# Optimization experiments

Hardware: AMD Instinct MI355X
Metric: run time of the kernel (lower is better)

Reference implementation:

```python
import jax, jax.numpy as jnp
import numpy as np

TEMP_LEN = 16
TARGET_LEN = 22
DIM = 768
HEADS = 12
B = 16
NT = TEMP_LEN * TEMP_LEN          # 256 template tokens
NG = TARGET_LEN * TARGET_LEN      # 484 target tokens
N = NT + NG                       # 740
POS_HID = 512


def _gaussian_heatmap(center, size, sig=1.0):
    x_axis = np.linspace(0, size[0] - 1, size[0]) - center[0]
    y_axis = np.linspace(0, size[1] - 1, size[1]) - center[1]
    xx, yy = np.meshgrid(x_axis, y_axis)
    return np.exp(-0.5 * (xx ** 2 + yy ** 2) / sig ** 2)


def _bias_index(L):
    # faithful to getBiasIndex (w_len == h_len here)
    coords = np.stack(np.meshgrid(np.arange(L), np.arange(L), indexing='ij'))  # [2,L,L]
    flat = coords.reshape(2, -1)                                               # [2,L*L]
    rel = (flat[:, :, None] - flat[:, None, :]).transpose(1, 2, 0).astype(np.int64)
    rel[:, :, 0] += L - 1
    rel[:, :, 1] += L - 1
    rel[:, :, 0] *= 2 * L - 1
    return rel.sum(-1)  # [L*L, L*L]


def setup_inputs() -> dict:
    key = jax.random.key(0)
    ks = jax.random.split(key, 12)
    f32 = jnp.float32
    x = jax.random.normal(ks[0], (B, N, DIM), dtype=f32)
    temp_q = jax.random.normal(ks[1], (B, NT, DIM), dtype=f32)
    target_q = jax.random.normal(ks[2], (B, NG, DIM), dtype=f32)
    # linear weights stored [in, out] (transposed torch layout)
    w = lambda k, i, o: jax.random.normal(k, (i, o), dtype=f32) * 0.02
    q_w = w(ks[3], DIM, DIM)
    k_w = w(ks[4], DIM, DIM)
    v_w = w(ks[5], DIM, DIM)
    proj_w = w(ks[6], DIM, DIM)
    proj_b = jnp.zeros((DIM,), dtype=f32)
    rpb_table = jax.random.normal(ks[7], ((2 * TARGET_LEN - 1) ** 2, HEADS), dtype=f32) * 0.0002
    rpb_table_temp = jax.random.normal(ks[8], ((2 * TEMP_LEN - 1) ** 2, HEADS), dtype=f32) * 0.0002
    pos_w1 = w(ks[9], 2, POS_HID)
    pos_b1 = jnp.zeros((POS_HID,), dtype=f32)
    pos_w2 = w(ks[10], POS_HID, HEADS)
    pos_b2 = jnp.zeros((HEADS,), dtype=f32)
    # deterministic cross-bias coordinate table (non-learned buffer)
    temp_tab = _gaussian_heatmap((TEMP_LEN // 2, TEMP_LEN // 2), (TEMP_LEN, TEMP_LEN)).astype(np.float32).flatten() \
        + np.linspace(-0.2, 0.2, NT, dtype=np.float32)
    targ_tab = _gaussian_heatmap((TARGET_LEN // 2, TARGET_LEN // 2), (TARGET_LEN, TARGET_LEN)).astype(np.float32).flatten() \
        + np.linspace(-0.2, 0.2, NG, dtype=np.float32)
    # torch.meshgrid default indexing='ij': [2, NT, NG] -> permute(1,2,0) -> [NT,NG,2]
    temp_target = np.stack(np.meshgrid(temp_tab, targ_tab, indexing='ij')).transpose(1, 2, 0)
    target_temp_tab = jnp.asarray(temp_target.transpose(1, 0, 2))  # [NG, NT, 2]
    temp_idx = jnp.asarray(_bias_index(TEMP_LEN))       # [NT, NT] int64
    target_idx = jnp.asarray(_bias_index(TARGET_LEN))   # [NG, NG] int64
    return {
        'x': x, 'temp_q': temp_q, 'target_q': target_q,
        'q_w': q_w, 'k_w': k_w, 'v_w': v_w, 'proj_w': proj_w, 'proj_b': proj_b,
        'rpb_table': rpb_table, 'rpb_table_temp': rpb_table_temp,
        'pos_w1': pos_w1, 'pos_b1': pos_b1, 'pos_w2': pos_w2, 'pos_b2': pos_b2,
        'target_temp_tab': target_temp_tab,
        'temp_idx': temp_idx, 'target_idx': target_idx,
    }


def reference(x, temp_q, target_q, q_w, k_w, v_w, proj_w, proj_b,
              rpb_table, rpb_table_temp, pos_w1, pos_b1, pos_w2, pos_b2,
              target_temp_tab, temp_idx, target_idx):
    Bsz, Ntok, C = x.shape
    H = HEADS
    hd = C // H
    scale = hd ** -0.5

    q_in = jnp.concatenate([temp_q, target_q], axis=1)                 # [B,N,C]
    q = (q_in @ q_w).reshape(Bsz, Ntok, H, hd).transpose(0, 2, 1, 3)   # [B,H,N,hd]
    k = (x @ k_w).reshape(Bsz, Ntok, H, hd).transpose(0, 2, 1, 3)
    v = (x @ v_w).reshape(Bsz, Ntok, H, hd).transpose(0, 2, 1, 3)

    # gathered relative position biases -> [H, Ni, Ni]
    temp_rpb = rpb_table_temp[temp_idx.reshape(-1)].reshape(NT, NT, H).transpose(2, 0, 1)
    targ_rpb = rpb_table[target_idx.reshape(-1)].reshape(NG, NG, H).transpose(2, 0, 1)
    # MLP cross bias: [NG, NT, 2] -> [NG, NT, H] -> [H, NG, NT]
    hid = jax.nn.relu(target_temp_tab @ pos_w1 + pos_b1)
    target_temp_bias = (hid @ pos_w2 + pos_b2).transpose(2, 0, 1)      # [H,NG,NT]
    temp_target_bias = target_temp_bias.transpose(0, 2, 1)             # [H,NT,NG]
    top = jnp.concatenate([temp_rpb, temp_target_bias], axis=2)        # [H,NT,N]
    bot = jnp.concatenate([target_temp_bias, targ_rpb], axis=2)        # [H,NG,N]
    bias = jnp.concatenate([top, bot], axis=1)[None]                   # [1,H,N,N]

    attn = jnp.einsum('bhnd,bhmd->bhnm', q, k) * scale + bias
    attn = jax.nn.softmax(attn, axis=-1)
    out = jnp.einsum('bhnm,bhmd->bhnd', attn, v).transpose(0, 2, 1, 3).reshape(Bsz, Ntok, C)
    return out @ proj_w + proj_b
```

## Files before the change

### kernel.cpp

```cpp
#include <hip/hip_runtime.h>


typedef unsigned short u16;
typedef short bf16x8 __attribute__((ext_vector_type(8)));
typedef float f32x4 __attribute__((ext_vector_type(4)));

#define BSZ   16
#define NTOK  740
#define NTMP  256
#define NTGT  484
#define DIMC  768
#define NHEAD 12
#define HDIM  64
#define MROWS (BSZ*NTOK)
#define SMAX  16.0f

__device__ __forceinline__ float bf2f(u16 u) {
    return __uint_as_float(((unsigned int)u) << 16);
}
__device__ __forceinline__ float bflo(unsigned int u) {
    return __uint_as_float(u << 16);
}
__device__ __forceinline__ float bfhi(unsigned int u) {
    return __uint_as_float(u & 0xffff0000u);
}
__device__ __forceinline__ u16 f2bf(float f) {
    unsigned int u = __float_as_uint(f);
    u += 0x7fffu + ((u >> 16) & 1u);
    return (u16)(u >> 16);
}

__device__ __forceinline__ void gl_lds16(const u16* g, u16* l) {
    __builtin_amdgcn_global_load_lds(
        (const __attribute__((address_space(1))) unsigned int*)(unsigned long long)g,
        (__attribute__((address_space(3))) unsigned int*)(unsigned int)(unsigned long long)l,
        16, 0, 0);
}

__device__ __forceinline__ size_t b2off(int h, int i, int j) {
    return ((size_t)(h * NTOK + i)) * 768 + ((j >> 6) << 6) + ((j & 15) << 2) + ((j >> 4) & 3);
}

#define PREP_CONV 4440
#define PREP_TRW  (PREP_CONV + 576)
#define PREP_DIAG (PREP_TRW + 2220)
#define PREP_ALL  (PREP_DIAG + 484)

__global__ __launch_bounds__(256) void prep_kernel(
    const float* __restrict__ x, const float* __restrict__ tq,
    const float* __restrict__ gq, u16* __restrict__ XB, u16* __restrict__ QB,
    const float* __restrict__ w0, const float* __restrict__ w1,
    const float* __restrict__ w2, const float* __restrict__ w3,
    u16* __restrict__ Wt,
    const float* __restrict__ rpb, const float* __restrict__ rpbt,
    const int* __restrict__ tidx, const int* __restrict__ gidx,
    const float* __restrict__ pw1, const float* __restrict__ pb1,
    const float* __restrict__ pw2, const float* __restrict__ pb2,
    const float* __restrict__ tab, u16* __restrict__ bias)
{
    __shared__ float T[64][65];
    const int blk = blockIdx.x;
    const int tid = threadIdx.x;

    if (blk < PREP_CONV) {
        int c = blk * 256 + tid;
        {
            const float* s = x + (size_t)c * 8;
            float4 p0 = *(const float4*)s, p1 = *(const float4*)(s + 4);
            u16 e[8] = {f2bf(p0.x), f2bf(p0.y), f2bf(p0.z), f2bf(p0.w),
                        f2bf(p1.x), f2bf(p1.y), f2bf(p1.z), f2bf(p1.w)};
            *(uint4*)(XB + (size_t)c * 8) = *(uint4*)e;
        }
        {
            int row = c / 96, cc = (c - row * 96) * 8;
            int b = row / NTOK, n = row - b * NTOK;
            const float* s = (n < NTMP)
                           ? tq + ((size_t)(b * NTMP + n)) * DIMC + cc
                           : gq + ((size_t)(b * NTGT + (n - NTMP))) * DIMC + cc;
            float4 p0 = *(const float4*)s, p1 = *(const float4*)(s + 4);
            u16 e[8] = {f2bf(p0.x), f2bf(p0.y), f2bf(p0.z), f2bf(p0.w),
                        f2bf(p1.x), f2bf(p1.y), f2bf(p1.z), f2bf(p1.w)};
            *(uint4*)(QB + (size_t)row * DIMC + cc) = *(uint4*)e;
        }
    } else if (blk < PREP_TRW) {
        int t = blk - PREP_CONV;
        int z = t / 144, rem = t - z * 144;
        int bx = rem % 12, by = rem / 12;
        const float* src = (z == 0) ? w0 : (z == 1) ? w1 : (z == 2) ? w2 : w3;
        const float scale = (z == 0) ? 0.125f : 1.0f;
        u16* dst = Wt + (size_t)z * DIMC * DIMC;
        int out0 = bx * 64, in0 = by * 64;
        #pragma unroll
        for (int l = 0; l < 4; l++) {
            int u = tid + (l << 8);
            int r = u >> 4, c4 = (u & 15) << 2;
            float4 p = *(const float4*)(src + (size_t)(in0 + r) * DIMC + out0 + c4);
            T[r][c4] = p.x; T[r][c4 + 1] = p.y; T[r][c4 + 2] = p.z; T[r][c4 + 3] = p.w;
        }
        __syncthreads();
        #pragma unroll
        for (int l = 0; l < 2; l++) {
            int u = tid + (l << 8);
            int r = u >> 3, c8 = (u & 7) << 3;
            u16 e[8];
            #pragma unroll
            for (int i = 0; i < 8; i++) e[i] = f2bf(T[c8 + i][r] * scale);
            *(uint4*)(dst + (size_t)(out0 + r) * DIMC + in0 + c8) = *(uint4*)e;
        }
    } else if (blk < PREP_DIAG) {
        int t = blk - PREP_TRW;
        int jb = t % 3, i = t / 3;
        int j = jb * 256 + tid;
        u16 vals[NHEAD];
        if (j >= NTOK) {
            u16 neg = f2bf(-1e30f);
            #pragma unroll
            for (int h = 0; h < NHEAD; h++) vals[h] = neg;
        } else if (i < NTMP && j < NTMP) {
            int idx = tidx[i * NTMP + j];
            #pragma unroll
            for (int h = 0; h < NHEAD; h++) vals[h] = f2bf(rpbt[idx * NHEAD + h]);
        } else if (i >= NTMP && j >= NTMP) {
            int idx = gidx[(i - NTMP) * NTGT + (j - NTMP)];
            #pragma unroll
            for (int h = 0; h < NHEAD; h++) vals[h] = f2bf(rpb[idx * NHEAD + h]);
        } else {
            return;
        }
        #pragma unroll
        for (int h = 0; h < NHEAD; h++) bias[b2off(h, i, j)] = vals[h];
    } else {
        int g = blk - PREP_DIAG;
        int t = tid;
        float a  = tab[(g * NTMP + t) * 2 + 0];
        float bb = tab[(g * NTMP + t) * 2 + 1];
        float acc[NHEAD];
        #pragma unroll
        for (int h = 0; h < NHEAD; h++) acc[h] = pb2[h];
        for (int k = 0; k < 512; k++) {
            float hid = fmaxf(a * pw1[k] + bb * pw1[512 + k] + pb1[k], 0.0f);
            #pragma unroll
            for (int h = 0; h < NHEAD; h++) acc[h] += hid * pw2[k * NHEAD + h];
        }
        #pragma unroll
        for (int h = 0; h < NHEAD; h++) {
            u16 v = f2bf(acc[h]);
            bias[b2off(h, t, NTMP + g)] = v;
            bias[b2off(h, NTMP + g, t)] = v;
        }
    }
}

template<int MODE>
__global__ __launch_bounds__(256) void gemm_bf16(
    const u16* __restrict__ A, const u16* __restrict__ Wt,
    const float* __restrict__ pb, u16* __restrict__ C0,
    u16* __restrict__ C1, float* __restrict__ Cf)
{
    __shared__ __align__(16) u16 As[2][8192];
    __shared__ __align__(16) u16 Bs[2][8192];
    const int tid = threadIdx.x;
    const int lane = tid & 63, w = tid >> 6;
    const int quad = lane >> 4, ln = lane & 15;

    const int gx = gridDim.x;
    const int nwg = gx * (int)gridDim.y;
    const int flat = blockIdx.y * gx + blockIdx.x;
    const int q = nwg >> 3, r = nwg & 7;
    const int xcd = flat & 7, sidx = flat >> 3;
    const int wg = (xcd < r) ? xcd * (q + 1) + sidx
                             : r * (q + 1) + (xcd - r) * q + sidx;
    const int by = wg / gx, bx = wg - by * gx;

    const int m0 = by << 7;
    const int wm = (w >> 1) << 6, wn = (w & 1) << 6;

    const int nn = bx << 7;
    const u16* Wbase = Wt + (size_t)nn * DIMC;
    u16* Cb;
    int col0;
    if (MODE == 1) {
        if (nn < DIMC) { col0 = nn; Cb = C0; }
        else           { col0 = nn - DIMC; Cb = C1; }
    } else {
        col0 = nn; Cb = C0;
    }

    f32x4 acc[4][4];
    #pragma unroll
    for (int i = 0; i < 4; i++)
        #pragma unroll
        for (int j = 0; j < 4; j++)
            acc[i][j] = (f32x4){0.f, 0.f, 0.f, 0.f};

#define STAGE(s, k0) do {                                                     \
    _Pragma("unroll")                                                         \
    for (int l = 0; l < 4; l++) {                                             \
        int f = tid + (l << 8);                                  \
        int c8 = f >> 7, rr = f & 127;                                        \
        int grow = m0 + rr; if (grow >= MROWS) grow = MROWS - 1;              \
        gl_lds16(A + (size_t)grow * DIMC + (k0) + c8 * 8, &As[s][f * 8]);     \
        gl_lds16(Wbase + (size_t)rr * DIMC + (k0) + c8 * 8, &Bs[s][f * 8]);   \
    } } while (0)

#define COMPUTE(s) do {                                                       \
    _Pragma("unroll")                                                         \
    for (int kp = 0; kp < 2; kp++) {                                          \
        bf16x8 af[4], bfr[4];                                                 \
        _Pragma("unroll")                                                     \
        for (int mt = 0; mt < 4; mt++)                                        \
            af[mt] = *(const bf16x8*)                                         \
                &As[s][(((kp << 2) + quad) * 128 + wm + mt * 16 + ln) * 8];   \
        _Pragma("unroll")                                                     \
        for (int nt = 0; nt < 4; nt++)                                        \
            bfr[nt] = *(const bf16x8*)                                        \
                &Bs[s][(((kp << 2) + quad) * 128 + wn + nt * 16 + ln) * 8];   \
        _Pragma("unroll")                                                     \
        for (int mt = 0; mt < 4; mt++)                                        \
            _Pragma("unroll")                                                 \
            for (int nt = 0; nt < 4; nt++)                                    \
                acc[mt][nt] = __builtin_amdgcn_mfma_f32_16x16x32_bf16(        \
                    af[mt], bfr[nt], acc[mt][nt], 0, 0, 0);                   \
    } } while (0)

    STAGE(0, 0);
    __syncthreads();
    #pragma unroll 1
    for (int t = 0; t < 12; t += 2) {
        STAGE(1, (t + 1) << 6);
        COMPUTE(0);
        __syncthreads();
        if (t < 10) STAGE(0, (t + 2) << 6);
        COMPUTE(1);
        __syncthreads();
    }

#undef STAGE
#undef COMPUTE

    #pragma unroll
    for (int mt = 0; mt < 4; mt++) {
        #pragma unroll
        for (int reg = 0; reg < 4; reg++) {
            int grow = m0 + wm + mt * 16 + (quad << 2) + reg;
            if (grow >= MROWS) continue;
            #pragma unroll
            for (int nt = 0; nt < 4; nt++) {
                int gcol = col0 + wn + nt * 16 + ln;
                float v = acc[mt][nt][reg];
                if (MODE == 2) {
                    Cf[(size_t)grow * DIMC + gcol] = v + pb[gcol];
                } else {
                    Cb[(size_t)grow * DIMC + gcol] = f2bf(v);
                }
            }
        }
    }
}

__global__ __launch_bounds__(256) void attn_mfma(
    const u16* __restrict__ Qg, const u16* __restrict__ Kg,
    const u16* __restrict__ Vg, const u16* __restrict__ bias,
    u16* __restrict__ ctx)
{
    __shared__ __align__(16) u16 KsL[4096];
    __shared__ __align__(16) u16 VtL[64 * 72];
    __shared__ __align__(16) u16 Pw[8][16][72];

    const int tid = threadIdx.x;
    const int lane = tid & 63, w = tid >> 6;
    const int quad = lane >> 4, ln = lane & 15;
    const int b = blockIdx.z, h = blockIdx.y;
    const int q0 = blockIdx.x << 7;
    const int mbase = q0 + (w << 5);
    const u16* bp = bias + ((size_t)h * NTOK) * 768;

    bf16x8 aq[2][2];
    #pragma unroll
    for (int mi = 0; mi < 2; mi++) {
        int qrow = mbase + (mi << 4) + ln; if (qrow >= NTOK) qrow = NTOK - 1;
        #pragma unroll
        for (int kp = 0; kp < 2; kp++)
            aq[mi][kp] = *(const bf16x8*)(Qg + ((size_t)(b * NTOK + qrow)) * DIMC
                                          + h * HDIM + kp * 32 + (quad << 3));
    }
    int boff[2][4];
    #pragma unroll
    for (int mi = 0; mi < 2; mi++)
        #pragma unroll
        for (int reg = 0; reg < 4; reg++) {
            int rr = mbase + (mi << 4) + (quad << 2) + reg;
            if (rr >= NTOK) rr = NTOK - 1;
            boff[mi][reg] = rr * 768 + (ln << 2);
        }

    const int pswz = ((ln >> 2) & 3) << 4;

    float rs[2][4] = {};
    f32x4 O[2][4];
    #pragma unroll
    for (int mi = 0; mi < 2; mi++)
        #pragma unroll
        for (int dt = 0; dt < 4; dt++) O[mi][dt] = (f32x4){0.f, 0.f, 0.f, 0.f};

    for (int j0 = 0; j0 < NTOK; j0 += 64) {
        __syncthreads();
        #pragma unroll
        for (int l = 0; l < 2; l++) {
            int f = tid + (l << 8);
            int chunk = f >> 6, jr = f & 63;
            int krow = j0 + jr; if (krow >= NTOK) krow = NTOK - 1;
            gl_lds16(Kg + ((size_t)(b * NTOK + krow)) * DIMC + h * HDIM + chunk * 8,
                     KsL + f * 8);
        }
        uint2 bvv[2][4];
        #pragma unroll
        for (int mi = 0; mi < 2; mi++)
            #pragma unroll
            for (int reg = 0; reg < 4; reg++)
                bvv[mi][reg] = *(const uint2*)(bp + boff[mi][reg] + j0);
        #pragma unroll
        for (int l = 0; l < 2; l++) {
            int u = tid + (l << 8);
            int jr = u >> 3, d0 = (u & 7) << 3;
            int vrow = j0 + jr; if (vrow >= NTOK) vrow = NTOK - 1;
            uint4 p = *(const uint4*)(Vg + ((size_t)(b * NTOK + vrow)) * DIMC + h * HDIM + d0);
            const u16* pe = (const u16*)&p;
            int jswz = jr ^ d0;
            #pragma unroll
            for (int i = 0; i < 8; i++) VtL[(d0 + i) * 72 + jswz] = pe[i];
        }
        __syncthreads();

        bf16x8 bv[4][2];
        #pragma unroll
        for (int dt = 0; dt < 4; dt++) {
            int key8 = ((dt * 2 + (ln >> 3)) & 7) << 3;
            #pragma unroll
            for (int kp = 0; kp < 2; kp++) {
                int koff = (kp * 32 + (quad << 3)) ^ key8;
                bv[dt][kp] = *(const bf16x8*)&VtL[(dt * 16 + ln) * 72 + koff];
            }
        }

        f32x4 s[2][4];
        #pragma unroll
        for (int mi = 0; mi < 2; mi++)
            #pragma unroll
            for (int nt = 0; nt < 4; nt++) s[mi][nt] = (f32x4){0.f, 0.f, 0.f, 0.f};
        #pragma unroll
        for (int kp = 0; kp < 2; kp++)
            #pragma unroll
            for (int nt = 0; nt < 4; nt++) {
                bf16x8 bk = *(const bf16x8*)
                    &KsL[(((kp << 2) + quad) * 64 + nt * 16 + ln) * 8];
                s[0][nt] = __builtin_amdgcn_mfma_f32_16x16x32_bf16(aq[0][kp], bk, s[0][nt], 0, 0, 0);
                s[1][nt] = __builtin_amdgcn_mfma_f32_16x16x32_bf16(aq[1][kp], bk, s[1][nt], 0, 0, 0);
            }

        #pragma unroll
        for (int mi = 0; mi < 2; mi++) {
            #pragma unroll
            for (int reg = 0; reg < 4; reg++) {
                uint2 bb = bvv[mi][reg];
                float p0 = __expf(s[mi][0][reg] + bflo(bb.x) - SMAX);
                float p1 = __expf(s[mi][1][reg] + bfhi(bb.x) - SMAX);
                float p2 = __expf(s[mi][2][reg] + bflo(bb.y) - SMAX);
                float p3 = __expf(s[mi][3][reg] + bfhi(bb.y) - SMAX);
                s[mi][0][reg] = p0; s[mi][1][reg] = p1;
                s[mi][2][reg] = p2; s[mi][3][reg] = p3;
                rs[mi][reg] += p0 + p1 + p2 + p3;
            }
            u16* pwb = &Pw[(w << 1) + mi][0][0];
            #pragma unroll
            for (int nt = 0; nt < 4; nt++) {
                int colw = ((nt ^ quad) << 4) + ln;
                #pragma unroll
                for (int reg = 0; reg < 4; reg++)
                    pwb[((quad << 2) + reg) * 72 + colw] = f2bf(s[mi][nt][reg]);
            }
            bf16x8 ap[2];
            #pragma unroll
            for (int kp = 0; kp < 2; kp++) {
                int koff = (kp * 32 + (quad << 3)) ^ pswz;
                ap[kp] = *(const bf16x8*)&pwb[ln * 72 + koff];
            }
            #pragma unroll
            for (int dt = 0; dt < 4; dt++)
                #pragma unroll
                for (int kp = 0; kp < 2; kp++)
                    O[mi][dt] = __builtin_amdgcn_mfma_f32_16x16x32_bf16(
                        ap[kp], bv[dt][kp], O[mi][dt], 0, 0, 0);
        }
    }

    #pragma unroll
    for (int mi = 0; mi < 2; mi++) {
        #pragma unroll
        for (int reg = 0; reg < 4; reg++) {
            float t = rs[mi][reg];
            #pragma unroll
            for (int mk = 8; mk >= 1; mk >>= 1) t += __shfl_xor(t, mk);
            float inv = 1.0f / t;
            int row = mbase + (mi << 4) + (quad << 2) + reg;
            if (row < NTOK) {
                #pragma unroll
                for (int dt = 0; dt < 4; dt++)
                    ctx[((size_t)(b * NTOK + row)) * DIMC + h * HDIM + dt * 16 + ln]
                        = f2bf(O[mi][dt][reg] * inv);
            }
        }
    }
}

extern "C" void kernel_launch(void* const* d_in, const int* in_sizes, int n_in,
                              void* d_out, int out_size, void* d_ws, size_t ws_size,
                              hipStream_t stream)
{
    const float* x        = (const float*)d_in[0];
    const float* temp_q   = (const float*)d_in[1];
    const float* target_q = (const float*)d_in[2];
    const float* q_w      = (const float*)d_in[3];
    const float* k_w      = (const float*)d_in[4];
    const float* v_w      = (const float*)d_in[5];
    const float* proj_w   = (const float*)d_in[6];
    const float* proj_b   = (const float*)d_in[7];
    const float* rpb      = (const float*)d_in[8];
    const float* rpbt     = (const float*)d_in[9];
    const float* pw1      = (const float*)d_in[10];
    const float* pb1      = (const float*)d_in[11];
    const float* pw2      = (const float*)d_in[12];
    const float* pb2      = (const float*)d_in[13];
    const float* tab      = (const float*)d_in[14];
    const int*   tidx     = (const int*)d_in[15];
    const int*   gidx     = (const int*)d_in[16];
    float* out = (float*)d_out;

    char* ws = (char*)d_ws;
    const size_t S = (size_t)MROWS * DIMC * sizeof(u16);
    const size_t SZB = (size_t)NHEAD * NTOK * 768 * sizeof(u16);
    u16* XB    = (u16*)(ws);
    u16* QB    = (u16*)(ws + S);
    u16* Q     = (u16*)(ws + 2 * S);
    u16* K     = (u16*)(ws + 3 * S);
    u16* V     = QB;
    u16* CTX   = XB;
    u16* BIAS2 = (u16*)(ws + 4 * S);
    u16* WT    = (u16*)(ws + 4 * S + SZB);

    prep_kernel<<<dim3(PREP_ALL), 256, 0, stream>>>(
        x, temp_q, target_q, XB, QB,
        q_w, k_w, v_w, proj_w, WT,
        rpb, rpbt, tidx, gidx,
        pw1, pb1, pw2, pb2, tab, BIAS2);

    const u16* WTq = WT;
    const u16* WTk = WT + (size_t)DIMC * DIMC;
    const u16* WTp = WT + 3 * (size_t)DIMC * DIMC;

    gemm_bf16<0><<<dim3(6, 93), 256, 0, stream>>>(QB, WTq, nullptr, Q, nullptr, nullptr);
    gemm_bf16<1><<<dim3(12, 93), 256, 0, stream>>>(XB, WTk, nullptr, K, V, nullptr);
    attn_mfma<<<dim3(6, 12, 16), 256, 0, stream>>>(Q, K, V, BIAS2, CTX);
    gemm_bf16<2><<<dim3(6, 93), 256, 0, stream>>>(CTX, WTp, proj_b, nullptr, nullptr, out);
}
```

Before: 469.4 us.

## Double-buffer K/V/bias tiles in attention and split bias MLP across blocks

The attention kernel now double-buffers the K and V LDS tiles and prefetches the next tile's K, V and bias while computing on the current one. This hides global-memory latency behind the MFMA work, and s_setprio is raised around the MFMA sections. The cross-bias MLP in the prep kernel is split into four k-slices per block with an LDS reduction and moved to the front of the grid, so its long serial blocks no longer trail the rest. The cost is more LDS and registers per attention block, which may lower occupancy.

```diff
diff --git a/kernel.cpp b/kernel.cpp
--- a/kernel.cpp
+++ b/kernel.cpp
@@ -41,10 +41,10 @@
     return ((size_t)(h * NTOK + i)) * 768 + ((j >> 6) << 6) + ((j & 15) << 2) + ((j >> 4) & 3);
 }
 
-#define PREP_CONV 4440
+#define PREP_MLP  1936
+#define PREP_CONV (PREP_MLP + 4440)
 #define PREP_TRW  (PREP_CONV + 576)
-#define PREP_DIAG (PREP_TRW + 2220)
-#define PREP_ALL  (PREP_DIAG + 484)
+#define PREP_ALL  (PREP_TRW + 2220)
 
 __global__ __launch_bounds__(256) void prep_kernel(
     const float* __restrict__ x, const float* __restrict__ tq,
@@ -62,8 +62,39 @@
     const int blk = blockIdx.x;
     const int tid = threadIdx.x;
 
-    if (blk < PREP_CONV) {
-        int c = blk * 256 + tid;
+    if (blk < PREP_MLP) {
+        int g  = blk >> 2;
+        int qt = blk & 3;
+        int tl = tid & 63, ks = tid >> 6;
+        int t  = (qt << 6) + tl;
+        float a  = tab[(g * NTMP + t) * 2 + 0];
+        float bb = tab[(g * NTMP + t) * 2 + 1];
+        float acc[NHEAD];
+        #pragma unroll
+        for (int h = 0; h < NHEAD; h++) acc[h] = 0.0f;
+        int k0 = ks << 7;
+        #pragma unroll 4
+        for (int k = k0; k < k0 + 128; k++) {
+            float hid = fmaxf(a * pw1[k] + bb * pw1[512 + k] + pb1[k], 0.0f);
+            #pragma unroll
+            for (int h = 0; h < NHEAD; h++) acc[h] += hid * pw2[k * NHEAD + h];
+        }
+        float* R = &T[0][0];
+        #pragma unroll
+        for (int h = 0; h < NHEAD; h++) R[(ks * 64 + tl) * 12 + h] = acc[h];
+        __syncthreads();
+        if (ks == 0) {
+            #pragma unroll
+            for (int h = 0; h < NHEAD; h++) {
+                float v = pb2[h] + R[tl * 12 + h] + R[(64 + tl) * 12 + h]
+                        + R[(128 + tl) * 12 + h] + R[(192 + tl) * 12 + h];
+                u16 u = f2bf(v);
+                bias[b2off(h, t, NTMP + g)] = u;
+                bias[b2off(h, NTMP + g, t)] = u;
+            }
+        }
+    } else if (blk < PREP_CONV) {
+        int c = (blk - PREP_MLP) * 256 + tid;
         {
             const float* s = x + (size_t)c * 8;
             float4 p0 = *(const float4*)s, p1 = *(const float4*)(s + 4);
@@ -107,7 +138,7 @@
             for (int i = 0; i < 8; i++) e[i] = f2bf(T[c8 + i][r] * scale);
             *(uint4*)(dst + (size_t)(out0 + r) * DIMC + in0 + c8) = *(uint4*)e;
         }
-    } else if (blk < PREP_DIAG) {
+    } else {
         int t = blk - PREP_TRW;
         int jb = t % 3, i = t / 3;
         int j = jb * 256 + tid;
@@ -129,25 +160,6 @@
         }
         #pragma unroll
         for (int h = 0; h < NHEAD; h++) bias[b2off(h, i, j)] = vals[h];
-    } else {
-        int g = blk - PREP_DIAG;
-        int t = tid;
-        float a  = tab[(g * NTMP + t) * 2 + 0];
-        float bb = tab[(g * NTMP + t) * 2 + 1];
-        float acc[NHEAD];
-        #pragma unroll
-        for (int h = 0; h < NHEAD; h++) acc[h] = pb2[h];
-        for (int k = 0; k < 512; k++) {
-            float hid = fmaxf(a * pw1[k] + bb * pw1[512 + k] + pb1[k], 0.0f);
-            #pragma unroll
-            for (int h = 0; h < NHEAD; h++) acc[h] += hid * pw2[k * NHEAD + h];
-        }
-        #pragma unroll
-        for (int h = 0; h < NHEAD; h++) {
-            u16 v = f2bf(acc[h]);
-            bias[b2off(h, t, NTMP + g)] = v;
-            bias[b2off(h, NTMP + g, t)] = v;
-        }
     }
 }
 
@@ -263,8 +275,8 @@
     const u16* __restrict__ Vg, const u16* __restrict__ bias,
     u16* __restrict__ ctx)
 {
-    __shared__ __align__(16) u16 KsL[4096];
-    __shared__ __align__(16) u16 VtL[64 * 72];
+    __shared__ __align__(16) u16 KsL[2][4096];
+    __shared__ __align__(16) u16 VtL[2][64 * 72];
     __shared__ __align__(16) u16 Pw[8][16][72];
 
     const int tid = threadIdx.x;
@@ -294,6 +306,13 @@
             boff[mi][reg] = rr * 768 + (ln << 2);
         }
 
+    int vjr[2], vd0[2];
+    #pragma unroll
+    for (int l = 0; l < 2; l++) {
+        int u = tid + (l << 8);
+        vjr[l] = u >> 3; vd0[l] = (u & 7) << 3;
+    }
+
     const int pswz = ((ln >> 2) & 3) << 4;
 
     float rs[2][4] = {};
@@ -303,34 +322,60 @@
         #pragma unroll
         for (int dt = 0; dt < 4; dt++) O[mi][dt] = (f32x4){0.f, 0.f, 0.f, 0.f};
 
-    for (int j0 = 0; j0 < NTOK; j0 += 64) {
-        __syncthreads();
-        #pragma unroll
-        for (int l = 0; l < 2; l++) {
-            int f = tid + (l << 8);
-            int chunk = f >> 6, jr = f & 63;
-            int krow = j0 + jr; if (krow >= NTOK) krow = NTOK - 1;
-            gl_lds16(Kg + ((size_t)(b * NTOK + krow)) * DIMC + h * HDIM + chunk * 8,
-                     KsL + f * 8);
-        }
-        uint2 bvv[2][4];
-        #pragma unroll
-        for (int mi = 0; mi < 2; mi++)
-            #pragma unroll
-            for (int reg = 0; reg < 4; reg++)
-                bvv[mi][reg] = *(const uint2*)(bp + boff[mi][reg] + j0);
-        #pragma unroll
-        for (int l = 0; l < 2; l++) {
-            int u = tid + (l << 8);
-            int jr = u >> 3, d0 = (u & 7) << 3;
-            int vrow = j0 + jr; if (vrow >= NTOK) vrow = NTOK - 1;
-            uint4 p = *(const uint4*)(Vg + ((size_t)(b * NTOK + vrow)) * DIMC + h * HDIM + d0);
-            const u16* pe = (const u16*)&p;
-            int jswz = jr ^ d0;
-            #pragma unroll
-            for (int i = 0; i < 8; i++) VtL[(d0 + i) * 72 + jswz] = pe[i];
-        }
-        __syncthreads();
+    uint4 vp[2];
+    uint2 bvv[2][4], bvn[2][4];
+
+#define STAGE_K(j0, s) do {                                                   \
+    _Pragma("unroll")                                                         \
+    for (int l = 0; l < 2; l++) {                                             \
+        int f = tid + (l << 8);                                               \
+        int chunk = f >> 6, jr = f & 63;                                      \
+        int krow = (j0) + jr; if (krow >= NTOK) krow = NTOK - 1;              \
+        gl_lds16(Kg + ((size_t)(b * NTOK + krow)) * DIMC + h * HDIM + chunk * 8, \
+                 &KsL[s][f * 8]);                                             \
+    } } while (0)
+
+#define LOAD_V(j0) do {                                                       \
+    _Pragma("unroll")                                                         \
+    for (int l = 0; l < 2; l++) {                                             \
+        int vrow = (j0) + vjr[l]; if (vrow >= NTOK) vrow = NTOK - 1;          \
+        vp[l] = *(const uint4*)(Vg + ((size_t)(b * NTOK + vrow)) * DIMC        \
+                                + h * HDIM + vd0[l]);                         \
+    } } while (0)
+
+#define WRITE_V(s) do {                                                       \
+    _Pragma("unroll")                                                         \
+    for (int l = 0; l < 2; l++) {                                             \
+        const u16* pe = (const u16*)&vp[l];                                   \
+        int jswz = vjr[l] ^ vd0[l];                                           \
+        _Pragma("unroll")                                                     \
+        for (int i = 0; i < 8; i++)                                           \
+            VtL[s][(vd0[l] + i) * 72 + jswz] = pe[i];                         \
+    } } while (0)
+
+#define LOAD_B(j0, dst) do {                                                  \
+    _Pragma("unroll")                                                         \
+    for (int mi = 0; mi < 2; mi++)                                            \
+        _Pragma("unroll")                                                     \
+        for (int reg = 0; reg < 4; reg++)                                     \
+            dst[mi][reg] = *(const uint2*)(bp + boff[mi][reg] + (j0));        \
+    } while (0)
+
+    STAGE_K(0, 0);
+    LOAD_V(0);
+    LOAD_B(0, bvv);
+    __syncthreads();
+    WRITE_V(0);
+    __syncthreads();
+
+    for (int tt = 0; tt < 12; tt++) {
+        const int p = tt & 1;
+        const int j0n = (tt + 1) << 6;
+        if (tt < 11) {
+            STAGE_K(j0n, p ^ 1);
+            LOAD_V(j0n);
+            LOAD_B(j0n, bvn);
+        }
 
         bf16x8 bv[4][2];
         #pragma unroll
@@ -339,7 +384,7 @@
             #pragma unroll
             for (int kp = 0; kp < 2; kp++) {
                 int koff = (kp * 32 + (quad << 3)) ^ key8;
-                bv[dt][kp] = *(const bf16x8*)&VtL[(dt * 16 + ln) * 72 + koff];
+                bv[dt][kp] = *(const bf16x8*)&VtL[p][(dt * 16 + ln) * 72 + koff];
             }
         }
 
@@ -348,15 +393,17 @@
         for (int mi = 0; mi < 2; mi++)
             #pragma unroll
             for (int nt = 0; nt < 4; nt++) s[mi][nt] = (f32x4){0.f, 0.f, 0.f, 0.f};
+        __builtin_amdgcn_s_setprio(1);
         #pragma unroll
         for (int kp = 0; kp < 2; kp++)
             #pragma unroll
             for (int nt = 0; nt < 4; nt++) {
                 bf16x8 bk = *(const bf16x8*)
-                    &KsL[(((kp << 2) + quad) * 64 + nt * 16 + ln) * 8];
+                    &KsL[p][(((kp << 2) + quad) * 64 + nt * 16 + ln) * 8];
                 s[0][nt] = __builtin_amdgcn_mfma_f32_16x16x32_bf16(aq[0][kp], bk, s[0][nt], 0, 0, 0);
                 s[1][nt] = __builtin_amdgcn_mfma_f32_16x16x32_bf16(aq[1][kp], bk, s[1][nt], 0, 0, 0);
             }
+        __builtin_amdgcn_s_setprio(0);
 
         #pragma unroll
         for (int mi = 0; mi < 2; mi++) {
@@ -385,14 +432,32 @@
                 int koff = (kp * 32 + (quad << 3)) ^ pswz;
                 ap[kp] = *(const bf16x8*)&pwb[ln * 72 + koff];
             }
+            __builtin_amdgcn_s_setprio(1);
             #pragma unroll
             for (int dt = 0; dt < 4; dt++)
                 #pragma unroll
                 for (int kp = 0; kp < 2; kp++)
                     O[mi][dt] = __builtin_amdgcn_mfma_f32_16x16x32_bf16(
                         ap[kp], bv[dt][kp], O[mi][dt], 0, 0, 0);
-        }
-    }
+            __builtin_amdgcn_s_setprio(0);
+        }
+
+        __syncthreads();
+        if (tt < 11) {
+            WRITE_V(p ^ 1);
+            #pragma unroll
+            for (int mi = 0; mi < 2; mi++)
+                #pragma unroll
+                for (int reg = 0; reg < 4; reg++)
+                    bvv[mi][reg] = bvn[mi][reg];
+            __syncthreads();
+        }
+    }
+
+#undef STAGE_K
+#undef LOAD_V
+#undef WRITE_V
+#undef LOAD_B
 
     #pragma unroll
     for (int mi = 0; mi < 2; mi++) {
```

Result: slower. 551.3 us (+17.5%).
